# Performance work log

Hardware: AMD Instinct MI355X
Metric: run time of the kernel (lower is better)

Reference implementation:

```python
import jax, jax.numpy as jnp
import numpy as np


def layer_norm(x, g, b, eps=1e-5):
    mu = jnp.mean(x, -1, keepdims=True)
    var = jnp.mean((x - mu) ** 2, -1, keepdims=True)
    return (x - mu) * jax.lax.rsqrt(var + eps) * g + b


def gru(x, h0, Wih, Whh, bih, bhh):
    """Single-layer torch-convention GRU. x:[B,T,E], h0:[B,H] -> (ys [B,T,H], h_last [B,H])."""
    xg = jnp.einsum('bte,ge->btg', x, Wih) + bih  # precompute input gates [B,T,3H]

    def step(h, xt):
        gh = h @ Whh.T + bhh
        xr, xz, xn = jnp.split(xt, 3, axis=-1)
        hr, hz, hn = jnp.split(gh, 3, axis=-1)
        r = jax.nn.sigmoid(xr + hr)
        z = jax.nn.sigmoid(xz + hz)
        n = jnp.tanh(xn + r * hn)
        h_new = (1.0 - z) * n + z * h
        return h_new, h_new

    h_last, ys = jax.lax.scan(step, h0, xg.transpose(1, 0, 2))
    return ys.transpose(1, 0, 2), h_last


def setup_inputs() -> dict:
    key = jax.random.key(0)
    ks = jax.random.split(key, 16)
    B, T, V, E, H, S, C = 16, 128, 32000, 300, 1024, 64, 192
    w = lambda k, shape: jax.random.normal(k, shape, jnp.float32) * 0.02
    return dict(
        x=jax.random.randint(ks[0], (B, T), 0, V),
        sos_token=jnp.ones((1,), jnp.int32),
        eps_s=jax.random.normal(ks[1], (1, B, S), jnp.float32),
        eps_c=jax.random.normal(ks[2], (1, B, C), jnp.float32),
        emb=w(ks[3], (V, E)),
        ln_g=jnp.ones((E,), jnp.float32), ln_b=jnp.zeros((E,), jnp.float32),
        enc_Wih=w(ks[4], (3 * H, E)), enc_Whh=w(ks[5], (3 * H, H)),
        enc_bih=jnp.zeros((3 * H,), jnp.float32), enc_bhh=jnp.zeros((3 * H,), jnp.float32),
        mus_W=w(ks[6], (S, H)), mus_b=jnp.zeros((S,), jnp.float32),
        vars_W=w(ks[7], (S, H)), vars_b=jnp.zeros((S,), jnp.float32),
        muc_W=w(ks[8], (C, H)), muc_b=jnp.zeros((C,), jnp.float32),
        varc_W=w(ks[9], (C, H)), varc_b=jnp.zeros((C,), jnp.float32),
        fc_W=w(ks[10], (H, S + C)), fc_b=jnp.zeros((H,), jnp.float32),
        dec_Wih=w(ks[11], (3 * H, E)), dec_Whh=w(ks[12], (3 * H, H)),
        dec_bih=jnp.zeros((3 * H,), jnp.float32), dec_bhh=jnp.zeros((3 * H,), jnp.float32),
        out_W=w(ks[13], (V, H)), out_b=jnp.zeros((V,), jnp.float32),
    )


def reference(x, sos_token, eps_s, eps_c, emb, ln_g, ln_b,
              enc_Wih, enc_Whh, enc_bih, enc_bhh,
              mus_W, mus_b, vars_W, vars_b, muc_W, muc_b, varc_W, varc_b,
              fc_W, fc_b, dec_Wih, dec_Whh, dec_bih, dec_bhh, out_W, out_b):
    B, T = x.shape
    H = enc_Whh.shape[1]
    e = layer_norm(emb[x], ln_g, ln_b)                            # [B,T,E]
    _, hn = gru(e, jnp.zeros((B, H), e.dtype), enc_Wih, enc_Whh, enc_bih, enc_bhh)
    hn = hn[None]                                                  # [1,B,H] (num_layers=1)
    mu_s = hn @ mus_W.T + mus_b
    logvar_s = hn @ vars_W.T + vars_b
    mu_c = hn @ muc_W.T + muc_b
    logvar_c = hn @ varc_W.T + varc_b
    style = mu_s + eps_s * jnp.exp(0.5 * logvar_s)
    content = mu_c + eps_c * jnp.exp(0.5 * logvar_c)
    z = jnp.concatenate([style, content], axis=-1) @ fc_W.T + fc_b  # [1,B,H]
    sos = layer_norm(emb[jnp.broadcast_to(sos_token[None, :], (B, 1))], ln_g, ln_b)  # [B,1,E]
    dec_in = jnp.concatenate([sos, e], axis=1)[:, :-1, :]          # [B,T,E]
    # Single scan == torch's O(T^2) prefix-recompute loop (same init state -> identical outputs)
    ys, _ = gru(dec_in, z[0], dec_Wih, dec_Whh, dec_bih, dec_bhh)  # [B,T,H]
    logits = jnp.einsum('bth,vh->btv', ys, out_W) + out_b          # [B,T,V]
    return logits, style, content, mu_s, logvar_s, mu_c, logvar_c
```

## Files before the change

kernel.cpp:

```cpp
#include <hip/hip_runtime.h>

#define B_  16
#define T_  128
#define E_  300
#define EP_ 320
#define H_  1024
#define G3_ 3072
#define V_  32000

typedef __attribute__((ext_vector_type(8))) short short8;
typedef __attribute__((ext_vector_type(4))) float floatx4;

#define OF_STYLE   65536000ull
#define OF_CONTENT 65537024ull
#define OF_MUS     65540096ull
#define OF_LVS     65541120ull
#define OF_MUC     65542144ull
#define OF_LVC     65545216ull

__device__ __forceinline__ unsigned short f2bf(float f) {
  union { float f; unsigned u; } v; v.f = f;
  return (unsigned short)((v.u + 0x7fffu + ((v.u >> 16) & 1u)) >> 16);
}

__device__ __forceinline__ float wsum(float v) {
  #pragma unroll
  for (int m = 1; m < 64; m <<= 1) v += __shfl_xor(v, m, 64);
  return v;
}

__device__ __forceinline__ float dot4(const float4 a, const float4 b) {
  return a.x * b.x + a.y * b.y + a.z * b.z + a.w * b.w;
}

__device__ __forceinline__ short8 cvt8(const float4 a, const float4 b) {
  short8 r;
  r[0] = (short)f2bf(a.x); r[1] = (short)f2bf(a.y);
  r[2] = (short)f2bf(a.z); r[3] = (short)f2bf(a.w);
  r[4] = (short)f2bf(b.x); r[5] = (short)f2bf(b.y);
  r[6] = (short)f2bf(b.z); r[7] = (short)f2bf(b.w);
  return r;
}

__global__ void k_wih(const float* __restrict__ src, unsigned short* __restrict__ dst) {
  int idx = blockIdx.x * 256 + threadIdx.x;
  const int stride = gridDim.x * 256;
  for (; idx < G3_ * EP_; idx += stride) {
    int row = idx / EP_;
    int k = idx - row * EP_;
    dst[idx] = (k < E_) ? f2bf(src[row * E_ + k]) : (unsigned short)0;
  }
}

__global__ void k_cvtw(const float* __restrict__ src, unsigned short* __restrict__ dst, int n4) {
  int i = blockIdx.x * 256 + threadIdx.x;
  const int stride = gridDim.x * 256;
  for (; i < n4; i += stride) {
    float4 f = ((const float4*)src)[i];
    union { unsigned short us[4]; unsigned long long u; } pk;
    pk.us[0] = f2bf(f.x); pk.us[1] = f2bf(f.y); pk.us[2] = f2bf(f.z); pk.us[3] = f2bf(f.w);
    ((unsigned long long*)dst)[i] = pk.u;
  }
}

__global__ void k_embed(const int* __restrict__ x, const int* __restrict__ sos,
                        const float* __restrict__ emb, const float* __restrict__ g,
                        const float* __restrict__ bta,
                        unsigned short* __restrict__ e2, unsigned short* __restrict__ de2) {
  const int row = blockIdx.x * 4 + (threadIdx.x >> 6);
  const int lane = threadIdx.x & 63;
  if (row > 2048) return;
  int tok, t = 0, b = 0;
  if (row < 2048) { b = row >> 7; t = row & 127; tok = x[row]; }
  else tok = sos[0];
  const float* src = emb + (size_t)tok * E_;
  float v[5]; float s = 0.f;
  #pragma unroll
  for (int i = 0; i < 5; ++i) { int k = lane + i * 64; v[i] = (k < E_) ? src[k] : 0.f; s += v[i]; }
  s = wsum(s);
  const float mu = s * (1.f / (float)E_);
  float q = 0.f;
  #pragma unroll
  for (int i = 0; i < 5; ++i) { int k = lane + i * 64; if (k < E_) { float d = v[i] - mu; q += d * d; } }
  q = wsum(q);
  const float rstd = rsqrtf(q * (1.f / (float)E_) + 1e-5f);
  #pragma unroll
  for (int i = 0; i < 5; ++i) {
    int k = lane + i * 64;
    unsigned short us = (k < E_) ? f2bf((v[i] - mu) * rstd * g[k] + bta[k]) : (unsigned short)0;
    if (row < 2048) {
      e2[(size_t)(t * 16 + b) * EP_ + k] = us;
      if (t < T_ - 1) de2[(size_t)((t + 1) * 16 + b) * EP_ + k] = us;
    } else {
      for (int bb = 0; bb < 16; ++bb) de2[(size_t)bb * EP_ + k] = us;
    }
  }
}

__global__ __launch_bounds__(256) void k_xg(const unsigned short* __restrict__ A,
                                            const unsigned short* __restrict__ Bm,
                                            const float* __restrict__ bih,
                                            float* __restrict__ xg) {
  __shared__ unsigned short lA[128 * 40];
  __shared__ unsigned short lB[128 * 40];
  const int tid = threadIdx.x;
  const int lane = tid & 63, wave = tid >> 6;
  const int wm = wave >> 1, wn = wave & 1;
  const int m0 = (blockIdx.x >> 4) * 128, n0 = (blockIdx.x & 15) * 128;
  floatx4 acc[4][4];
  #pragma unroll
  for (int i = 0; i < 4; ++i)
    #pragma unroll
    for (int jj = 0; jj < 4; ++jj) acc[i][jj] = (floatx4){0.f, 0.f, 0.f, 0.f};
  for (int kt = 0; kt < 10; ++kt) {
    const int k0 = kt * 32;
    __syncthreads();
    #pragma unroll
    for (int gi = 0; gi < 2; ++gi) {
      int gidx = tid + gi * 256;
      int r = gidx >> 2, kc = gidx & 3;
      short8 va = *(const short8*)(A + (size_t)(m0 + r) * EP_ + k0 + kc * 8);
      *(short8*)(&lA[r * 40 + kc * 8]) = va;
      short8 vb = *(const short8*)(Bm + (size_t)(n0 + r) * EP_ + k0 + kc * 8);
      *(short8*)(&lB[r * 40 + kc * 8]) = vb;
    }
    __syncthreads();
    short8 aF[4], bF[4];
    #pragma unroll
    for (int ms = 0; ms < 4; ++ms)
      aF[ms] = *(const short8*)(&lA[(wm * 64 + ms * 16 + (lane & 15)) * 40 + ((lane >> 4) << 3)]);
    #pragma unroll
    for (int ns = 0; ns < 4; ++ns)
      bF[ns] = *(const short8*)(&lB[(wn * 64 + ns * 16 + (lane & 15)) * 40 + ((lane >> 4) << 3)]);
    #pragma unroll
    for (int ms = 0; ms < 4; ++ms)
      #pragma unroll
      for (int ns = 0; ns < 4; ++ns)
        acc[ms][ns] = __builtin_amdgcn_mfma_f32_16x16x32_bf16(aF[ms], bF[ns], acc[ms][ns], 0, 0, 0);
  }
  #pragma unroll
  for (int ms = 0; ms < 4; ++ms) {
    const int mg0 = m0 + wm * 64 + ms * 16 + ((lane >> 4) << 2);
    #pragma unroll
    for (int ns = 0; ns < 4; ++ns) {
      const int nn = n0 + wn * 64 + ns * 16 + (lane & 15);
      const int tt = nn >> 4, bb = nn & 15;
      #pragma unroll
      for (int r = 0; r < 4; ++r)
        xg[(size_t)tt * (G3_ * 16) + (size_t)(mg0 + r) * 16 + bb] = acc[ms][ns][r] + bih[mg0 + r];
    }
  }
}

__global__ __launch_bounds__(256) void k_final(const unsigned short* __restrict__ Ay,
                                               const float* __restrict__ Bw,
                                               const float* __restrict__ obias,
                                               float* __restrict__ out) {
  __shared__ unsigned short lA[128 * 40];
  __shared__ unsigned short lB[128 * 40];
  const int tid = threadIdx.x;
  const int lane = tid & 63, wave = tid >> 6;
  const int wm = wave >> 1, wn = wave & 1;
  const int m0 = (blockIdx.x & 15) * 128, n0 = (blockIdx.x >> 4) * 128;
  floatx4 acc[4][4];
  #pragma unroll
  for (int i = 0; i < 4; ++i)
    #pragma unroll
    for (int jj = 0; jj < 4; ++jj) acc[i][jj] = (floatx4){0.f, 0.f, 0.f, 0.f};
  for (int kt = 0; kt < 32; ++kt) {
    const int k0 = kt * 32;
    __syncthreads();
    #pragma unroll
    for (int gi = 0; gi < 2; ++gi) {
      int gidx = tid + gi * 256;
      int r = gidx >> 2, kc = gidx & 3;
      short8 va = *(const short8*)(Ay + (size_t)(m0 + r) * H_ + k0 + kc * 8);
      *(short8*)(&lA[r * 40 + kc * 8]) = va;
    }
    #pragma unroll
    for (int gi = 0; gi < 4; ++gi) {
      int gidx = tid + gi * 256;
      int r = gidx >> 3, kc = gidx & 7;
      float4 f = *(const float4*)(Bw + (size_t)(n0 + r) * H_ + k0 + kc * 4);
      union { unsigned short us[4]; unsigned long long u; } pk;
      pk.us[0] = f2bf(f.x); pk.us[1] = f2bf(f.y); pk.us[2] = f2bf(f.z); pk.us[3] = f2bf(f.w);
      *(unsigned long long*)(&lB[r * 40 + kc * 4]) = pk.u;
    }
    __syncthreads();
    short8 aF[4], bF[4];
    #pragma unroll
    for (int ms = 0; ms < 4; ++ms)
      aF[ms] = *(const short8*)(&lA[(wm * 64 + ms * 16 + (lane & 15)) * 40 + ((lane >> 4) << 3)]);
    #pragma unroll
    for (int ns = 0; ns < 4; ++ns)
      bF[ns] = *(const short8*)(&lB[(wn * 64 + ns * 16 + (lane & 15)) * 40 + ((lane >> 4) << 3)]);
    #pragma unroll
    for (int ms = 0; ms < 4; ++ms)
      #pragma unroll
      for (int ns = 0; ns < 4; ++ns)
        acc[ms][ns] = __builtin_amdgcn_mfma_f32_16x16x32_bf16(aF[ms], bF[ns], acc[ms][ns], 0, 0, 0);
  }
  #pragma unroll
  for (int ns = 0; ns < 4; ++ns) {
    const int nn = n0 + wn * 64 + ns * 16 + (lane & 15);
    const float bs = obias[nn];
    #pragma unroll
    for (int ms = 0; ms < 4; ++ms) {
      const int mm = m0 + wm * 64 + ms * 16 + ((lane >> 4) << 2);
      #pragma unroll
      for (int r = 0; r < 4; ++r)
        out[(size_t)(mm + r) * V_ + nn] = acc[ms][ns][r] + bs;
    }
  }
}

__global__ __launch_bounds__(256) void k_final_bf(const unsigned short* __restrict__ Ay,
                                                  const unsigned short* __restrict__ Bw,
                                                  const float* __restrict__ obias,
                                                  float* __restrict__ out) {
  __shared__ unsigned short lA[128 * 40];
  __shared__ unsigned short lB[128 * 40];
  const int tid = threadIdx.x;
  const int lane = tid & 63, wave = tid >> 6;
  const int wm = wave >> 1, wn = wave & 1;
  const int m0 = (blockIdx.x & 15) * 128, n0 = (blockIdx.x >> 4) * 128;
  floatx4 acc[4][4];
  #pragma unroll
  for (int i = 0; i < 4; ++i)
    #pragma unroll
    for (int jj = 0; jj < 4; ++jj) acc[i][jj] = (floatx4){0.f, 0.f, 0.f, 0.f};
  for (int kt = 0; kt < 32; ++kt) {
    const int k0 = kt * 32;
    __syncthreads();
    #pragma unroll
    for (int gi = 0; gi < 2; ++gi) {
      int gidx = tid + gi * 256;
      int r = gidx >> 2, kc = gidx & 3;
      short8 va = *(const short8*)(Ay + (size_t)(m0 + r) * H_ + k0 + kc * 8);
      *(short8*)(&lA[r * 40 + kc * 8]) = va;
      short8 vb = *(const short8*)(Bw + (size_t)(n0 + r) * H_ + k0 + kc * 8);
      *(short8*)(&lB[r * 40 + kc * 8]) = vb;
    }
    __syncthreads();
    short8 aF[4], bF[4];
    #pragma unroll
    for (int ms = 0; ms < 4; ++ms)
      aF[ms] = *(const short8*)(&lA[(wm * 64 + ms * 16 + (lane & 15)) * 40 + ((lane >> 4) << 3)]);
    #pragma unroll
    for (int ns = 0; ns < 4; ++ns)
      bF[ns] = *(const short8*)(&lB[(wn * 64 + ns * 16 + (lane & 15)) * 40 + ((lane >> 4) << 3)]);
    #pragma unroll
    for (int ms = 0; ms < 4; ++ms)
      #pragma unroll
      for (int ns = 0; ns < 4; ++ns)
        acc[ms][ns] = __builtin_amdgcn_mfma_f32_16x16x32_bf16(aF[ms], bF[ns], acc[ms][ns], 0, 0, 0);
  }
  #pragma unroll
  for (int ns = 0; ns < 4; ++ns) {
    const int nn = n0 + wn * 64 + ns * 16 + (lane & 15);
    const float bs = obias[nn];
    #pragma unroll
    for (int ms = 0; ms < 4; ++ms) {
      const int mm = m0 + wm * 64 + ms * 16 + ((lane >> 4) << 2);
      #pragma unroll
      for (int r = 0; r < 4; ++r)
        out[(size_t)(mm + r) * V_ + nn] = acc[ms][ns][r] + bs;
    }
  }
}

__global__ __launch_bounds__(256, 1) void k_gru(const float* __restrict__ xg,
                                                const float* __restrict__ Whh,
                                                const float* __restrict__ bhh,
                                                const float* __restrict__ h0,
                                                unsigned long long* hbuf, int* flags,
                                                float* __restrict__ hn_out,
                                                unsigned short* __restrict__ ys) {
  __shared__ float lred[3072];
  const int tid = threadIdx.x;
  const int lane = tid & 63, wave = tid >> 6;
  const int j = blockIdx.x;
  const int b = tid & 15, c = tid >> 4;
  const int hc = j * 16 + c;
  const int kbase = wave * 256;

  short8 bfrag[3][8];
  #pragma unroll
  for (int tau = 0; tau < 3; ++tau) {
    const float* wr = Whh + (size_t)(tau * H_ + j * 16 + (lane & 15)) * H_;
    #pragma unroll
    for (int s8 = 0; s8 < 8; ++s8) {
      int k = kbase + s8 * 32 + ((lane >> 4) << 3);
      float4 p0 = *(const float4*)(wr + k);
      float4 p1 = *(const float4*)(wr + k + 4);
      bfrag[tau][s8] = cvt8(p0, p1);
    }
  }
  const float bh0 = bhh[hc], bh1 = bhh[H_ + hc], bh2 = bhh[2 * H_ + hc];
  float h_own = h0 ? h0[b * H_ + hc] : 0.f;

  #define PACK_STORE(HVAL, BUF)                                                              \
    {                                                                                        \
      unsigned wlo = f2bf(HVAL);                                                             \
      unsigned p = wlo | (((unsigned)__shfl_xor((int)wlo, 16, 64)) << 16);                   \
      unsigned long long qv = (unsigned long long)p |                                        \
          (((unsigned long long)(unsigned)__shfl_xor((int)p, 32, 64)) << 32);                \
      if (lane < 16)                                                                         \
        __hip_atomic_store(hbuf + (size_t)(BUF) * 4096 + (j * 4 + wave) * 16 + lane, qv,     \
                           __ATOMIC_RELAXED, __HIP_MEMORY_SCOPE_AGENT);                      \
    }

  PACK_STORE(h_own, 0)
  float xr = xg[hc * 16 + b];
  float xz = xg[(H_ + hc) * 16 + b];
  float xn = xg[(2 * H_ + hc) * 16 + b];
  __syncthreads();
  if (tid == 0) __hip_atomic_store(flags + j, 1, __ATOMIC_RELAXED, __HIP_MEMORY_SCOPE_AGENT);
  if (wave == 0) {
    for (;;) {
      int f = __hip_atomic_load(flags + lane, __ATOMIC_RELAXED, __HIP_MEMORY_SCOPE_AGENT);
      if (__all(f >= 1)) break;
      __builtin_amdgcn_s_sleep(1);
    }
  }
  __syncthreads();

  for (int s = 0; s < T_; ++s) {
    const unsigned long long* src = hbuf + (size_t)(s & 1) * 4096;
    unsigned long long qa0[8], qa1[8];
    #pragma unroll
    for (int s8 = 0; s8 < 8; ++s8) {
      const int qi = (wave * 64 + s8 * 8 + ((lane >> 4) << 1)) * 16 + (lane & 15);
      qa0[s8] = __hip_atomic_load(src + qi,      __ATOMIC_RELAXED, __HIP_MEMORY_SCOPE_AGENT);
      qa1[s8] = __hip_atomic_load(src + qi + 16, __ATOMIC_RELAXED, __HIP_MEMORY_SCOPE_AGENT);
    }
    floatx4 a0 = {0.f,0.f,0.f,0.f}, a1 = {0.f,0.f,0.f,0.f}, a2 = {0.f,0.f,0.f,0.f};
    #pragma unroll
    for (int s8 = 0; s8 < 8; ++s8) {
      union { unsigned long long q[2]; short8 v; } u;
      u.q[0] = qa0[s8]; u.q[1] = qa1[s8];
      a0 = __builtin_amdgcn_mfma_f32_16x16x32_bf16(u.v, bfrag[0][s8], a0, 0, 0, 0);
      a1 = __builtin_amdgcn_mfma_f32_16x16x32_bf16(u.v, bfrag[1][s8], a1, 0, 0, 0);
      a2 = __builtin_amdgcn_mfma_f32_16x16x32_bf16(u.v, bfrag[2][s8], a2, 0, 0, 0);
    }
    {
      int pb = wave * 768 + (lane & 15) * 16 + ((lane >> 4) << 2);
      *(floatx4*)(&lred[pb])       = a0;
      *(floatx4*)(&lred[pb + 256]) = a1;
      *(floatx4*)(&lred[pb + 512]) = a2;
    }
    __syncthreads();
    float g0 = bh0, g1 = bh1, g2 = bh2;
    #pragma unroll
    for (int wv = 0; wv < 4; ++wv) {
      int rb = wv * 768 + c * 16 + b;
      g0 += lred[rb]; g1 += lred[rb + 256]; g2 += lred[rb + 512];
    }
    const float rg = 1.f / (1.f + expf(-(xr + g0)));
    const float zg = 1.f / (1.f + expf(-(xz + g1)));
    const float ng = tanhf(xn + rg * g2);
    const float hnew = (1.f - zg) * ng + zg * h_own;
    h_own = hnew;
    if (ys) ys[(size_t)(b * T_ + s) * H_ + hc] = f2bf(hnew);
    PACK_STORE(hnew, (s + 1) & 1)
    if (s < T_ - 1) {
      const float* xgn = xg + (size_t)(s + 1) * (G3_ * 16);
      float xrN = xgn[hc * 16 + b];
      float xzN = xgn[(H_ + hc) * 16 + b];
      float xnN = xgn[(2 * H_ + hc) * 16 + b];
      __syncthreads();
      if (tid == 0) __hip_atomic_store(flags + j, s + 2, __ATOMIC_RELAXED, __HIP_MEMORY_SCOPE_AGENT);
      if (wave == 0) {
        for (;;) {
          int f = __hip_atomic_load(flags + lane, __ATOMIC_RELAXED, __HIP_MEMORY_SCOPE_AGENT);
          if (__all(f >= s + 2)) break;
          __builtin_amdgcn_s_sleep(1);
        }
      }
      __syncthreads();
      xr = xrN; xz = xzN; xn = xnN;
    }
  }
  if (hn_out) hn_out[b * H_ + hc] = h_own;
  #undef PACK_STORE
}

__global__ void k_heads(const float* __restrict__ hn,
                        const float* __restrict__ musW, const float* __restrict__ musb,
                        const float* __restrict__ varsW, const float* __restrict__ varsb,
                        const float* __restrict__ mucW, const float* __restrict__ mucb,
                        const float* __restrict__ varcW, const float* __restrict__ varcb,
                        const float* __restrict__ eps_s, const float* __restrict__ eps_c,
                        float* __restrict__ out, float* __restrict__ cat) {
  const int wv = blockIdx.x * 4 + (threadIdx.x >> 6);
  const int lane = threadIdx.x & 63;
  const int b = wv >> 8, o = wv & 255;
  const float* h = hn + (size_t)b * H_;
  const float *w1, *w2; float bb1, bb2, ep; int oc = 0;
  const int smode = (o < 64);
  if (smode) { w1 = musW + (size_t)o * H_;  w2 = varsW + (size_t)o * H_;  bb1 = musb[o];  bb2 = varsb[o];  ep = eps_s[b * 64 + o]; }
  else { oc = o - 64; w1 = mucW + (size_t)oc * H_; w2 = varcW + (size_t)oc * H_; bb1 = mucb[oc]; bb2 = varcb[oc]; ep = eps_c[b * 192 + oc]; }
  float s1 = 0.f, s2 = 0.f;
  #pragma unroll
  for (int i = 0; i < 4; ++i) {
    int k = lane * 4 + i * 256;
    float4 hv = *(const float4*)(h + k);
    float4 av = *(const float4*)(w1 + k);
    float4 bv = *(const float4*)(w2 + k);
    s1 += dot4(hv, av); s2 += dot4(hv, bv);
  }
  s1 = wsum(s1); s2 = wsum(s2);
  if (lane == 0) {
    const float mu = s1 + bb1, lv = s2 + bb2;
    const float sc = mu + ep * expf(0.5f * lv);
    if (smode) {
      out[OF_MUS + b * 64 + o] = mu;
      out[OF_LVS + b * 64 + o] = lv;
      out[OF_STYLE + b * 64 + o] = sc;
      cat[b * 256 + o] = sc;
    } else {
      out[OF_MUC + b * 192 + oc] = mu;
      out[OF_LVC + b * 192 + oc] = lv;
      out[OF_CONTENT + b * 192 + oc] = sc;
      cat[b * 256 + 64 + oc] = sc;
    }
  }
}

__global__ void k_z(const float* __restrict__ cat, const float* __restrict__ fcW,
                    const float* __restrict__ fcb, float* __restrict__ z) {
  const int wv = blockIdx.x * 4 + (threadIdx.x >> 6);
  const int lane = threadIdx.x & 63;
  const int b = wv >> 10, h = wv & 1023;
  float4 a = *(const float4*)(cat + b * 256 + lane * 4);
  float4 w = *(const float4*)(fcW + (size_t)h * 256 + lane * 4);
  float p = dot4(a, w);
  p = wsum(p);
  if (lane == 0) z[b * H_ + h] = p + fcb[h];
}

extern "C" void kernel_launch(void* const* d_in, const int* in_sizes, int n_in,
                              void* d_out, int out_size, void* d_ws, size_t ws_size,
                              hipStream_t stream) {
  (void)in_sizes; (void)n_in; (void)out_size;
  const int*   x       = (const int*)d_in[0];
  const int*   sos     = (const int*)d_in[1];
  const float* eps_s   = (const float*)d_in[2];
  const float* eps_c   = (const float*)d_in[3];
  const float* emb     = (const float*)d_in[4];
  const float* ln_g    = (const float*)d_in[5];
  const float* ln_b    = (const float*)d_in[6];
  const float* enc_Wih = (const float*)d_in[7];
  const float* enc_Whh = (const float*)d_in[8];
  const float* enc_bih = (const float*)d_in[9];
  const float* enc_bhh = (const float*)d_in[10];
  const float* mus_W   = (const float*)d_in[11];
  const float* mus_b   = (const float*)d_in[12];
  const float* vars_W  = (const float*)d_in[13];
  const float* vars_b  = (const float*)d_in[14];
  const float* muc_W   = (const float*)d_in[15];
  const float* muc_b   = (const float*)d_in[16];
  const float* varc_W  = (const float*)d_in[17];
  const float* varc_b  = (const float*)d_in[18];
  const float* fc_W    = (const float*)d_in[19];
  const float* fc_b    = (const float*)d_in[20];
  const float* dec_Wih = (const float*)d_in[21];
  const float* dec_Whh = (const float*)d_in[22];
  const float* dec_bih = (const float*)d_in[23];
  const float* dec_bhh = (const float*)d_in[24];
  const float* out_W   = (const float*)d_in[25];
  const float* out_b   = (const float*)d_in[26];
  float* out = (float*)d_out;

  char* w = (char*)d_ws;
  unsigned short* e2   = (unsigned short*)(w + 0);
  unsigned short* de2  = (unsigned short*)(w + 1310720);
  unsigned short* wihE = (unsigned short*)(w + 2621440);
  unsigned short* wihD = (unsigned short*)(w + 4587520);
  float* xgE           = (float*)(w + 6553600);
  float* xgD           = (float*)(w + 31719424);
  unsigned short* ys   = (unsigned short*)(w + 56885248);
  unsigned long long* hbuf = (unsigned long long*)(w + 61079552);
  float* hn            = (float*)(w + 61145088);
  float* zb            = (float*)(w + 61210624);
  float* catb          = (float*)(w + 61276160);
  int* flagsE          = (int*)(w + 61292544);
  int* flagsD          = flagsE + 64;
  unsigned short* woutBf = (unsigned short*)(w + 61293056);
  const bool bigws = (ws_size >= 126829056ull);

  k_wih<<<960, 256, 0, stream>>>(enc_Wih, wihE);
  k_wih<<<960, 256, 0, stream>>>(dec_Wih, wihD);
  if (bigws) k_cvtw<<<2048, 256, 0, stream>>>(out_W, woutBf, V_ * H_ / 4);
  k_embed<<<513, 256, 0, stream>>>(x, sos, emb, ln_g, ln_b, e2, de2);
  k_xg<<<384, 256, 0, stream>>>(wihE, e2, enc_bih, xgE);
  k_xg<<<384, 256, 0, stream>>>(wihD, de2, dec_bih, xgD);
  k_gru<<<64, 256, 0, stream>>>(xgE, enc_Whh, enc_bhh, (const float*)nullptr,
                                hbuf, flagsE, hn, (unsigned short*)nullptr);
  k_heads<<<1024, 256, 0, stream>>>(hn, mus_W, mus_b, vars_W, vars_b,
                                    muc_W, muc_b, varc_W, varc_b, eps_s, eps_c, out, catb);
  k_z<<<4096, 256, 0, stream>>>(catb, fc_W, fc_b, zb);
  k_gru<<<64, 256, 0, stream>>>(xgD, dec_Whh, dec_bhh, zb,
                                hbuf, flagsD, (float*)nullptr, ys);
  if (bigws) k_final_bf<<<4000, 256, 0, stream>>>(ys, woutBf, out_b, out);
  else       k_final<<<4000, 256, 0, stream>>>(ys, out_W, out_b, out);
}
```

Baseline: 1.686 ms.

## Replace GRU flag barrier with per-element tagged hidden-state polling

Each hidden-state element now carries a 16-bit step tag in the upper half of a 32-bit word, so consumer waves spin directly on the data they need instead of waiting on a separate per-block flag array and two block barriers each step. The LDS reduction buffer is double-buffered so the trailing __syncthreads can be removed. The hidden buffer is relocated into the workspace region previously used by wihE (which is already consumed by then). This removes a grid-wide barrier round trip per timestep but doubles the hidden-state traffic and relies on the tag check being race-free.

```diff
diff --git a/kernel.cpp b/kernel.cpp
--- a/kernel.cpp
+++ b/kernel.cpp
@@ -17,6 +17,8 @@
 #define OF_LVS     65541120ull
 #define OF_MUC     65542144ull
 #define OF_LVC     65545216ull
+
+#define TAGB 0xFF00u
 
 __device__ __forceinline__ unsigned short f2bf(float f) {
   union { float f; unsigned u; } v; v.f = f;
@@ -273,10 +275,10 @@
                                                 const float* __restrict__ Whh,
                                                 const float* __restrict__ bhh,
                                                 const float* __restrict__ h0,
-                                                unsigned long long* hbuf, int* flags,
+                                                unsigned int* hbuf,
                                                 float* __restrict__ hn_out,
                                                 unsigned short* __restrict__ ys) {
-  __shared__ float lred[3072];
+  __shared__ float lred[2][3072];
   const int tid = threadIdx.x;
   const int lane = tid & 63, wave = tid >> 6;
   const int j = blockIdx.x;
@@ -284,6 +286,11 @@
   const int hc = j * 16 + c;
   const int kbase = wave * 256;
 
+  float h_own = h0 ? h0[b * H_ + hc] : 0.f;
+  __hip_atomic_store(hbuf + (size_t)b * 1024 + hc,
+                     (unsigned)f2bf(h_own) | (TAGB << 16),
+                     __ATOMIC_RELAXED, __HIP_MEMORY_SCOPE_AGENT);
+
   short8 bfrag[3][8];
   #pragma unroll
   for (int tau = 0; tau < 3; ++tau) {
@@ -297,92 +304,78 @@
     }
   }
   const float bh0 = bhh[hc], bh1 = bhh[H_ + hc], bh2 = bhh[2 * H_ + hc];
-  float h_own = h0 ? h0[b * H_ + hc] : 0.f;
-
-  #define PACK_STORE(HVAL, BUF)                                                              \
-    {                                                                                        \
-      unsigned wlo = f2bf(HVAL);                                                             \
-      unsigned p = wlo | (((unsigned)__shfl_xor((int)wlo, 16, 64)) << 16);                   \
-      unsigned long long qv = (unsigned long long)p |                                        \
-          (((unsigned long long)(unsigned)__shfl_xor((int)p, 32, 64)) << 32);                \
-      if (lane < 16)                                                                         \
-        __hip_atomic_store(hbuf + (size_t)(BUF) * 4096 + (j * 4 + wave) * 16 + lane, qv,     \
-                           __ATOMIC_RELAXED, __HIP_MEMORY_SCOPE_AGENT);                      \
-    }
-
-  PACK_STORE(h_own, 0)
+
   float xr = xg[hc * 16 + b];
   float xz = xg[(H_ + hc) * 16 + b];
   float xn = xg[(2 * H_ + hc) * 16 + b];
-  __syncthreads();
-  if (tid == 0) __hip_atomic_store(flags + j, 1, __ATOMIC_RELAXED, __HIP_MEMORY_SCOPE_AGENT);
-  if (wave == 0) {
+
+  const int rrow = lane & 15;
+  const int rcolb = kbase + ((lane >> 4) << 3);
+  const unsigned long long* qbase =
+      (const unsigned long long*)hbuf + ((size_t)rrow << 9) + (rcolb >> 1);
+
+  for (int s = 0; s < T_; ++s) {
+    const unsigned long long* src = qbase + ((size_t)(s & 1) << 13);
+    const unsigned exp16 = TAGB + (unsigned)s;
+    const unsigned long long expq =
+        ((unsigned long long)exp16 << 16) | ((unsigned long long)exp16 << 48);
+    unsigned long long q[8][4];
     for (;;) {
-      int f = __hip_atomic_load(flags + lane, __ATOMIC_RELAXED, __HIP_MEMORY_SCOPE_AGENT);
-      if (__all(f >= 1)) break;
+      bool ok = true;
+      #pragma unroll
+      for (int s8 = 0; s8 < 8; ++s8)
+        #pragma unroll
+        for (int p = 0; p < 4; ++p) {
+          q[s8][p] = __hip_atomic_load(src + s8 * 16 + p,
+                                       __ATOMIC_RELAXED, __HIP_MEMORY_SCOPE_AGENT);
+          ok &= ((q[s8][p] & 0xFFFF0000FFFF0000ull) == expq);
+        }
+      if (__all(ok)) break;
       __builtin_amdgcn_s_sleep(1);
     }
-  }
-  __syncthreads();
-
-  for (int s = 0; s < T_; ++s) {
-    const unsigned long long* src = hbuf + (size_t)(s & 1) * 4096;
-    unsigned long long qa0[8], qa1[8];
+    floatx4 a0 = {0.f,0.f,0.f,0.f}, a1 = {0.f,0.f,0.f,0.f}, a2 = {0.f,0.f,0.f,0.f};
     #pragma unroll
     for (int s8 = 0; s8 < 8; ++s8) {
-      const int qi = (wave * 64 + s8 * 8 + ((lane >> 4) << 1)) * 16 + (lane & 15);
-      qa0[s8] = __hip_atomic_load(src + qi,      __ATOMIC_RELAXED, __HIP_MEMORY_SCOPE_AGENT);
-      qa1[s8] = __hip_atomic_load(src + qi + 16, __ATOMIC_RELAXED, __HIP_MEMORY_SCOPE_AGENT);
-    }
-    floatx4 a0 = {0.f,0.f,0.f,0.f}, a1 = {0.f,0.f,0.f,0.f}, a2 = {0.f,0.f,0.f,0.f};
-    #pragma unroll
-    for (int s8 = 0; s8 < 8; ++s8) {
-      union { unsigned long long q[2]; short8 v; } u;
-      u.q[0] = qa0[s8]; u.q[1] = qa1[s8];
-      a0 = __builtin_amdgcn_mfma_f32_16x16x32_bf16(u.v, bfrag[0][s8], a0, 0, 0, 0);
-      a1 = __builtin_amdgcn_mfma_f32_16x16x32_bf16(u.v, bfrag[1][s8], a1, 0, 0, 0);
-      a2 = __builtin_amdgcn_mfma_f32_16x16x32_bf16(u.v, bfrag[2][s8], a2, 0, 0, 0);
-    }
+      union { unsigned u[4]; short8 v; } uu;
+      #pragma unroll
+      for (int p = 0; p < 4; ++p)
+        uu.u[p] = (unsigned)(q[s8][p] & 0xffffu) |
+                  ((unsigned)(q[s8][p] >> 16) & 0xffff0000u);
+      a0 = __builtin_amdgcn_mfma_f32_16x16x32_bf16(uu.v, bfrag[0][s8], a0, 0, 0, 0);
+      a1 = __builtin_amdgcn_mfma_f32_16x16x32_bf16(uu.v, bfrag[1][s8], a1, 0, 0, 0);
+      a2 = __builtin_amdgcn_mfma_f32_16x16x32_bf16(uu.v, bfrag[2][s8], a2, 0, 0, 0);
+    }
+    float* lr = lred[s & 1];
     {
       int pb = wave * 768 + (lane & 15) * 16 + ((lane >> 4) << 2);
-      *(floatx4*)(&lred[pb])       = a0;
-      *(floatx4*)(&lred[pb + 256]) = a1;
-      *(floatx4*)(&lred[pb + 512]) = a2;
+      *(floatx4*)(&lr[pb])       = a0;
+      *(floatx4*)(&lr[pb + 256]) = a1;
+      *(floatx4*)(&lr[pb + 512]) = a2;
     }
     __syncthreads();
     float g0 = bh0, g1 = bh1, g2 = bh2;
     #pragma unroll
     for (int wv = 0; wv < 4; ++wv) {
       int rb = wv * 768 + c * 16 + b;
-      g0 += lred[rb]; g1 += lred[rb + 256]; g2 += lred[rb + 512];
+      g0 += lr[rb]; g1 += lr[rb + 256]; g2 += lr[rb + 512];
     }
     const float rg = 1.f / (1.f + expf(-(xr + g0)));
     const float zg = 1.f / (1.f + expf(-(xz + g1)));
     const float ng = tanhf(xn + rg * g2);
     const float hnew = (1.f - zg) * ng + zg * h_own;
     h_own = hnew;
+    __hip_atomic_store(hbuf + ((size_t)((s + 1) & 1) << 14) + (size_t)b * 1024 + hc,
+                       (unsigned)f2bf(hnew) | ((TAGB + (unsigned)(s + 1)) << 16),
+                       __ATOMIC_RELAXED, __HIP_MEMORY_SCOPE_AGENT);
     if (ys) ys[(size_t)(b * T_ + s) * H_ + hc] = f2bf(hnew);
-    PACK_STORE(hnew, (s + 1) & 1)
     if (s < T_ - 1) {
       const float* xgn = xg + (size_t)(s + 1) * (G3_ * 16);
-      float xrN = xgn[hc * 16 + b];
-      float xzN = xgn[(H_ + hc) * 16 + b];
-      float xnN = xgn[(2 * H_ + hc) * 16 + b];
-      __syncthreads();
-      if (tid == 0) __hip_atomic_store(flags + j, s + 2, __ATOMIC_RELAXED, __HIP_MEMORY_SCOPE_AGENT);
-      if (wave == 0) {
-        for (;;) {
-          int f = __hip_atomic_load(flags + lane, __ATOMIC_RELAXED, __HIP_MEMORY_SCOPE_AGENT);
-          if (__all(f >= s + 2)) break;
-          __builtin_amdgcn_s_sleep(1);
-        }
-      }
-      __syncthreads();
-      xr = xrN; xz = xzN; xn = xnN;
+      xr = xgn[hc * 16 + b];
+      xz = xgn[(H_ + hc) * 16 + b];
+      xn = xgn[(2 * H_ + hc) * 16 + b];
     }
   }
   if (hn_out) hn_out[b * H_ + hc] = h_own;
-  #undef PACK_STORE
 }
 
 __global__ void k_heads(const float* __restrict__ hn,
@@ -480,13 +473,12 @@
   float* xgE           = (float*)(w + 6553600);
   float* xgD           = (float*)(w + 31719424);
   unsigned short* ys   = (unsigned short*)(w + 56885248);
-  unsigned long long* hbuf = (unsigned long long*)(w + 61079552);
   float* hn            = (float*)(w + 61145088);
   float* zb            = (float*)(w + 61210624);
   float* catb          = (float*)(w + 61276160);
-  int* flagsE          = (int*)(w + 61292544);
-  int* flagsD          = flagsE + 64;
   unsigned short* woutBf = (unsigned short*)(w + 61293056);
+  unsigned int* hbufE  = (unsigned int*)(w + 2621440);
+  unsigned int* hbufD  = (unsigned int*)(w + 2621440 + 131072);
   const bool bigws = (ws_size >= 126829056ull);
 
   k_wih<<<960, 256, 0, stream>>>(enc_Wih, wihE);
@@ -496,12 +488,12 @@
   k_xg<<<384, 256, 0, stream>>>(wihE, e2, enc_bih, xgE);
   k_xg<<<384, 256, 0, stream>>>(wihD, de2, dec_bih, xgD);
   k_gru<<<64, 256, 0, stream>>>(xgE, enc_Whh, enc_bhh, (const float*)nullptr,
-                                hbuf, flagsE, hn, (unsigned short*)nullptr);
+                                hbufE, hn, (unsigned short*)nullptr);
   k_heads<<<1024, 256, 0, stream>>>(hn, mus_W, mus_b, vars_W, vars_b,
                                     muc_W, muc_b, varc_W, varc_b, eps_s, eps_c, out, catb);
   k_z<<<4096, 256, 0, stream>>>(catb, fc_W, fc_b, zb);
   k_gru<<<64, 256, 0, stream>>>(xgD, dec_Whh, dec_bhh, zb,
-                                hbuf, flagsD, (float*)nullptr, ys);
+                                hbufD, (float*)nullptr, ys);
   if (bigws) k_final_bf<<<4000, 256, 0, stream>>>(ys, woutBf, out_b, out);
   else       k_final<<<4000, 256, 0, stream>>>(ys, out_W, out_b, out);
 }
```

Result: slower. 2.476 ms (+46.8%).

## Overlap GRU recurrences with independent GEMMs and the streamed output projection

Applied to the files above, without the earlier changes.

The encoder GRU kernel is fused with the decoder input-gate GEMM and the out_W bf16 conversion, so those blocks run on the idle CUs during the 64-block sequential recurrence. The decoder GRU is fused with the vocab projection GEMM: projection blocks spin on the per-block step flags until the ys rows they need are written, then compute, so the logits GEMM streams behind the recurrence. ys is relaid out time-major with sc1 stores, and the output row index is remapped to match. This depends on all GRU blocks being resident and scheduled before the waiting blocks, or it can deadlock. Spinning blocks may also take CU resources from the recurrence, which gets raised wave priority to offset this.

```diff
diff --git a/kernel.cpp b/kernel.cpp
--- a/kernel.cpp
+++ b/kernel.cpp
@@ -42,6 +42,10 @@
   return r;
 }
 
+__device__ __forceinline__ void st2_sc1(unsigned short* p, unsigned short v) {
+  asm volatile("global_store_short %0, %1, off sc1" :: "v"(p), "v"((unsigned)v) : "memory");
+}
+
 __global__ void k_wih(const float* __restrict__ src, unsigned short* __restrict__ dst) {
   int idx = blockIdx.x * 256 + threadIdx.x;
   const int stride = gridDim.x * 256;
@@ -49,17 +53,6 @@
     int row = idx / EP_;
     int k = idx - row * EP_;
     dst[idx] = (k < E_) ? f2bf(src[row * E_ + k]) : (unsigned short)0;
-  }
-}
-
-__global__ void k_cvtw(const float* __restrict__ src, unsigned short* __restrict__ dst, int n4) {
-  int i = blockIdx.x * 256 + threadIdx.x;
-  const int stride = gridDim.x * 256;
-  for (; i < n4; i += stride) {
-    float4 f = ((const float4*)src)[i];
-    union { unsigned short us[4]; unsigned long long u; } pk;
-    pk.us[0] = f2bf(f.x); pk.us[1] = f2bf(f.y); pk.us[2] = f2bf(f.z); pk.us[3] = f2bf(f.w);
-    ((unsigned long long*)dst)[i] = pk.u;
   }
 }
 
@@ -97,16 +90,16 @@
   }
 }
 
-__global__ __launch_bounds__(256) void k_xg(const unsigned short* __restrict__ A,
-                                            const unsigned short* __restrict__ Bm,
-                                            const float* __restrict__ bih,
-                                            float* __restrict__ xg) {
-  __shared__ unsigned short lA[128 * 40];
-  __shared__ unsigned short lB[128 * 40];
-  const int tid = threadIdx.x;
+__device__ __forceinline__ void xg_body(const int bid,
+                                        const unsigned short* __restrict__ A,
+                                        const unsigned short* __restrict__ Bm,
+                                        const float* __restrict__ bih,
+                                        float* __restrict__ xg,
+                                        unsigned short* lA, unsigned short* lB,
+                                        const int tid) {
   const int lane = tid & 63, wave = tid >> 6;
   const int wm = wave >> 1, wn = wave & 1;
-  const int m0 = (blockIdx.x >> 4) * 128, n0 = (blockIdx.x & 15) * 128;
+  const int m0 = (bid >> 4) * 128, n0 = (bid & 15) * 128;
   floatx4 acc[4][4];
   #pragma unroll
   for (int i = 0; i < 4; ++i)
@@ -148,6 +141,73 @@
       #pragma unroll
       for (int r = 0; r < 4; ++r)
         xg[(size_t)tt * (G3_ * 16) + (size_t)(mg0 + r) * 16 + bb] = acc[ms][ns][r] + bih[mg0 + r];
+    }
+  }
+}
+
+__global__ __launch_bounds__(256) void k_xg(const unsigned short* __restrict__ A,
+                                            const unsigned short* __restrict__ Bm,
+                                            const float* __restrict__ bih,
+                                            float* __restrict__ xg) {
+  __shared__ unsigned short lA[128 * 40];
+  __shared__ unsigned short lB[128 * 40];
+  xg_body(blockIdx.x, A, Bm, bih, xg, lA, lB, threadIdx.x);
+}
+
+__device__ __forceinline__ void final_bf_body(const int fbid,
+                                              const unsigned short* __restrict__ Ay,
+                                              const unsigned short* __restrict__ Bw,
+                                              const float* __restrict__ obias,
+                                              float* __restrict__ out,
+                                              unsigned short* lA, unsigned short* lB,
+                                              const int tid) {
+  const int lane = tid & 63, wave = tid >> 6;
+  const int wm = wave >> 1, wn = wave & 1;
+  const int m0 = (fbid & 15) * 128, n0 = (fbid >> 4) * 128;
+  floatx4 acc[4][4];
+  #pragma unroll
+  for (int i = 0; i < 4; ++i)
+    #pragma unroll
+    for (int jj = 0; jj < 4; ++jj) acc[i][jj] = (floatx4){0.f, 0.f, 0.f, 0.f};
+  for (int kt = 0; kt < 32; ++kt) {
+    const int k0 = kt * 32;
+    __syncthreads();
+    #pragma unroll
+    for (int gi = 0; gi < 2; ++gi) {
+      int gidx = tid + gi * 256;
+      int r = gidx >> 2, kc = gidx & 3;
+      short8 va = *(const short8*)(Ay + (size_t)(m0 + r) * H_ + k0 + kc * 8);
+      *(short8*)(&lA[r * 40 + kc * 8]) = va;
+      short8 vb = *(const short8*)(Bw + (size_t)(n0 + r) * H_ + k0 + kc * 8);
+      *(short8*)(&lB[r * 40 + kc * 8]) = vb;
+    }
+    __syncthreads();
+    short8 aF[4], bF[4];
+    #pragma unroll
+    for (int ms = 0; ms < 4; ++ms)
+      aF[ms] = *(const short8*)(&lA[(wm * 64 + ms * 16 + (lane & 15)) * 40 + ((lane >> 4) << 3)]);
+    #pragma unroll
+    for (int ns = 0; ns < 4; ++ns)
+      bF[ns] = *(const short8*)(&lB[(wn * 64 + ns * 16 + (lane & 15)) * 40 + ((lane >> 4) << 3)]);
+    #pragma unroll
+    for (int ms = 0; ms < 4; ++ms)
+      #pragma unroll
+      for (int ns = 0; ns < 4; ++ns)
+        acc[ms][ns] = __builtin_amdgcn_mfma_f32_16x16x32_bf16(aF[ms], bF[ns], acc[ms][ns], 0, 0, 0);
+  }
+  #pragma unroll
+  for (int ns = 0; ns < 4; ++ns) {
+    const int nn = n0 + wn * 64 + ns * 16 + (lane & 15);
+    const float bs = obias[nn];
+    #pragma unroll
+    for (int ms = 0; ms < 4; ++ms) {
+      const int mm = m0 + wm * 64 + ms * 16 + ((lane >> 4) << 2);
+      #pragma unroll
+      for (int r = 0; r < 4; ++r) {
+        const int q = mm + r;
+        const int orow = (q & 15) * 128 + (q >> 4);
+        out[(size_t)orow * V_ + nn] = acc[ms][ns][r] + bs;
+      }
     }
   }
 }
@@ -208,81 +268,28 @@
     for (int ms = 0; ms < 4; ++ms) {
       const int mm = m0 + wm * 64 + ms * 16 + ((lane >> 4) << 2);
       #pragma unroll
-      for (int r = 0; r < 4; ++r)
-        out[(size_t)(mm + r) * V_ + nn] = acc[ms][ns][r] + bs;
-    }
-  }
-}
-
-__global__ __launch_bounds__(256) void k_final_bf(const unsigned short* __restrict__ Ay,
-                                                  const unsigned short* __restrict__ Bw,
-                                                  const float* __restrict__ obias,
-                                                  float* __restrict__ out) {
-  __shared__ unsigned short lA[128 * 40];
-  __shared__ unsigned short lB[128 * 40];
-  const int tid = threadIdx.x;
+      for (int r = 0; r < 4; ++r) {
+        const int q = mm + r;
+        const int orow = (q & 15) * 128 + (q >> 4);
+        out[(size_t)orow * V_ + nn] = acc[ms][ns][r] + bs;
+      }
+    }
+  }
+}
+
+__device__ __forceinline__ void gru_body(const float* __restrict__ xg,
+                                         const float* __restrict__ Whh,
+                                         const float* __restrict__ bhh,
+                                         const float* __restrict__ h0,
+                                         unsigned long long* hbuf, int* flags,
+                                         float* __restrict__ hn_out,
+                                         unsigned short* __restrict__ ys,
+                                         float* lred, const int j, const int tid) {
   const int lane = tid & 63, wave = tid >> 6;
-  const int wm = wave >> 1, wn = wave & 1;
-  const int m0 = (blockIdx.x & 15) * 128, n0 = (blockIdx.x >> 4) * 128;
-  floatx4 acc[4][4];
-  #pragma unroll
-  for (int i = 0; i < 4; ++i)
-    #pragma unroll
-    for (int jj = 0; jj < 4; ++jj) acc[i][jj] = (floatx4){0.f, 0.f, 0.f, 0.f};
-  for (int kt = 0; kt < 32; ++kt) {
-    const int k0 = kt * 32;
-    __syncthreads();
-    #pragma unroll
-    for (int gi = 0; gi < 2; ++gi) {
-      int gidx = tid + gi * 256;
-      int r = gidx >> 2, kc = gidx & 3;
-      short8 va = *(const short8*)(Ay + (size_t)(m0 + r) * H_ + k0 + kc * 8);
-      *(short8*)(&lA[r * 40 + kc * 8]) = va;
-      short8 vb = *(const short8*)(Bw + (size_t)(n0 + r) * H_ + k0 + kc * 8);
-      *(short8*)(&lB[r * 40 + kc * 8]) = vb;
-    }
-    __syncthreads();
-    short8 aF[4], bF[4];
-    #pragma unroll
-    for (int ms = 0; ms < 4; ++ms)
-      aF[ms] = *(const short8*)(&lA[(wm * 64 + ms * 16 + (lane & 15)) * 40 + ((lane >> 4) << 3)]);
-    #pragma unroll
-    for (int ns = 0; ns < 4; ++ns)
-      bF[ns] = *(const short8*)(&lB[(wn * 64 + ns * 16 + (lane & 15)) * 40 + ((lane >> 4) << 3)]);
-    #pragma unroll
-    for (int ms = 0; ms < 4; ++ms)
-      #pragma unroll
-      for (int ns = 0; ns < 4; ++ns)
-        acc[ms][ns] = __builtin_amdgcn_mfma_f32_16x16x32_bf16(aF[ms], bF[ns], acc[ms][ns], 0, 0, 0);
-  }
-  #pragma unroll
-  for (int ns = 0; ns < 4; ++ns) {
-    const int nn = n0 + wn * 64 + ns * 16 + (lane & 15);
-    const float bs = obias[nn];
-    #pragma unroll
-    for (int ms = 0; ms < 4; ++ms) {
-      const int mm = m0 + wm * 64 + ms * 16 + ((lane >> 4) << 2);
-      #pragma unroll
-      for (int r = 0; r < 4; ++r)
-        out[(size_t)(mm + r) * V_ + nn] = acc[ms][ns][r] + bs;
-    }
-  }
-}
-
-__global__ __launch_bounds__(256, 1) void k_gru(const float* __restrict__ xg,
-                                                const float* __restrict__ Whh,
-                                                const float* __restrict__ bhh,
-                                                const float* __restrict__ h0,
-                                                unsigned long long* hbuf, int* flags,
-                                                float* __restrict__ hn_out,
-                                                unsigned short* __restrict__ ys) {
-  __shared__ float lred[3072];
-  const int tid = threadIdx.x;
-  const int lane = tid & 63, wave = tid >> 6;
-  const int j = blockIdx.x;
   const int b = tid & 15, c = tid >> 4;
   const int hc = j * 16 + c;
   const int kbase = wave * 256;
+  __builtin_amdgcn_s_setprio(3);
 
   short8 bfrag[3][8];
   #pragma unroll
@@ -361,7 +368,7 @@
     const float ng = tanhf(xn + rg * g2);
     const float hnew = (1.f - zg) * ng + zg * h_own;
     h_own = hnew;
-    if (ys) ys[(size_t)(b * T_ + s) * H_ + hc] = f2bf(hnew);
+    if (ys) st2_sc1(ys + (size_t)(s * 16 + b) * H_ + hc, f2bf(hnew));
     PACK_STORE(hnew, (s + 1) & 1)
     if (s < T_ - 1) {
       const float* xgn = xg + (size_t)(s + 1) * (G3_ * 16);
@@ -381,8 +388,66 @@
       xr = xrN; xz = xzN; xn = xnN;
     }
   }
+  __syncthreads();
+  if (tid == 0) __hip_atomic_store(flags + j, T_ + 2, __ATOMIC_RELAXED, __HIP_MEMORY_SCOPE_AGENT);
   if (hn_out) hn_out[b * H_ + hc] = h_own;
   #undef PACK_STORE
+}
+
+__global__ __launch_bounds__(256, 1) void k_gruE_fused(
+    const float* __restrict__ xg, const float* __restrict__ Whh,
+    const float* __restrict__ bhh,
+    unsigned long long* hbuf, int* flags, float* __restrict__ hn_out,
+    const unsigned short* __restrict__ A2, const unsigned short* __restrict__ B2,
+    const float* __restrict__ bih2, float* __restrict__ xg2,
+    const float* __restrict__ cvsrc, unsigned short* __restrict__ cvdst, int n4) {
+  __shared__ float lred[3072];
+  __shared__ unsigned short lA[128 * 40];
+  __shared__ unsigned short lB[128 * 40];
+  const int tid = threadIdx.x;
+  const int bid = blockIdx.x;
+  if (bid < 64) {
+    gru_body(xg, Whh, bhh, nullptr, hbuf, flags, hn_out, nullptr, lred, bid, tid);
+  } else if (bid < 448) {
+    xg_body(bid - 64, A2, B2, bih2, xg2, lA, lB, tid);
+  } else {
+    int i = (bid - 448) * 256 + tid;
+    const int stride = 512 * 256;
+    for (; i < n4; i += stride) {
+      float4 f = ((const float4*)cvsrc)[i];
+      union { unsigned short us[4]; unsigned long long u; } pk;
+      pk.us[0] = f2bf(f.x); pk.us[1] = f2bf(f.y); pk.us[2] = f2bf(f.z); pk.us[3] = f2bf(f.w);
+      ((unsigned long long*)cvdst)[i] = pk.u;
+    }
+  }
+}
+
+__global__ __launch_bounds__(256, 1) void k_gruD_fused(
+    const float* __restrict__ xg, const float* __restrict__ Whh,
+    const float* __restrict__ bhh, const float* __restrict__ h0,
+    unsigned long long* hbuf, int* flags, unsigned short* __restrict__ ys,
+    const unsigned short* __restrict__ Bw, const float* __restrict__ obias,
+    float* __restrict__ out) {
+  __shared__ float lred[3072];
+  __shared__ unsigned short lA[128 * 40];
+  __shared__ unsigned short lB[128 * 40];
+  const int tid = threadIdx.x;
+  const int bid = blockIdx.x;
+  if (bid < 64) {
+    gru_body(xg, Whh, bhh, h0, hbuf, flags, nullptr, ys, lred, bid, tid);
+  } else {
+    const int fbid = bid - 64;
+    const int need = (fbid & 15) * 8 + 9;
+    if (tid < 64) {
+      for (;;) {
+        int f = __hip_atomic_load(flags + tid, __ATOMIC_RELAXED, __HIP_MEMORY_SCOPE_AGENT);
+        if (__all(f >= need)) break;
+        __builtin_amdgcn_s_sleep(127);
+      }
+    }
+    __syncthreads();
+    final_bf_body(fbid, ys, Bw, obias, out, lA, lB, tid);
+  }
 }
 
 __global__ void k_heads(const float* __restrict__ hn,
@@ -491,17 +556,22 @@
 
   k_wih<<<960, 256, 0, stream>>>(enc_Wih, wihE);
   k_wih<<<960, 256, 0, stream>>>(dec_Wih, wihD);
-  if (bigws) k_cvtw<<<2048, 256, 0, stream>>>(out_W, woutBf, V_ * H_ / 4);
   k_embed<<<513, 256, 0, stream>>>(x, sos, emb, ln_g, ln_b, e2, de2);
   k_xg<<<384, 256, 0, stream>>>(wihE, e2, enc_bih, xgE);
-  k_xg<<<384, 256, 0, stream>>>(wihD, de2, dec_bih, xgD);
-  k_gru<<<64, 256, 0, stream>>>(xgE, enc_Whh, enc_bhh, (const float*)nullptr,
-                                hbuf, flagsE, hn, (unsigned short*)nullptr);
+  k_gruE_fused<<<bigws ? 960 : 448, 256, 0, stream>>>(
+      xgE, enc_Whh, enc_bhh, hbuf, flagsE, hn,
+      wihD, de2, dec_bih, xgD,
+      out_W, bigws ? woutBf : (unsigned short*)nullptr, V_ * H_ / 4);
   k_heads<<<1024, 256, 0, stream>>>(hn, mus_W, mus_b, vars_W, vars_b,
                                     muc_W, muc_b, varc_W, varc_b, eps_s, eps_c, out, catb);
   k_z<<<4096, 256, 0, stream>>>(catb, fc_W, fc_b, zb);
-  k_gru<<<64, 256, 0, stream>>>(xgD, dec_Whh, dec_bhh, zb,
-                                hbuf, flagsD, (float*)nullptr, ys);
-  if (bigws) k_final_bf<<<4000, 256, 0, stream>>>(ys, woutBf, out_b, out);
-  else       k_final<<<4000, 256, 0, stream>>>(ys, out_W, out_b, out);
-}
+  if (bigws) {
+    k_gruD_fused<<<64 + 4000, 256, 0, stream>>>(
+        xgD, dec_Whh, dec_bhh, zb, hbuf, flagsD, ys, woutBf, out_b, out);
+  } else {
+    k_gruD_fused<<<64, 256, 0, stream>>>(
+        xgD, dec_Whh, dec_bhh, zb, hbuf, flagsD, ys,
+        (const unsigned short*)nullptr, out_b, out);
+    k_final<<<4000, 256, 0, stream>>>(ys, out_W, out_b, out);
+  }
+}
```

Result: slower. 1.816 ms (+7.7%).
